# Kernel optimization log

Hardware: AMD Instinct MI355X
Metric: run time of the kernel (lower is better)

The kernel has to match this reference:

```python
import jax, jax.numpy as jnp
import numpy as np

REGION1 = REGION2 = 64
OVERLAP1 = OVERLAP2 = 0
MAX_M1 = MAX_M2 = 16


def dht1(x, axis):
    # 1D discrete Hartley transform along `axis` (real - imag of FFT)
    X = jnp.fft.fft(x, axis=axis)
    return X.real - X.imag


def dht2(x):
    # 2D DHT over last two axes
    X = jnp.fft.fft2(x, axes=(-2, -1))
    return X.real - X.imag


def flip_periodic2(x):
    # Faithful to torch code: flatten last two dims jointly, keep element 0, flip the rest
    s = x.shape
    n = s[-2] * s[-1]
    xf = x.reshape(s[:-2] + (n,))
    zf = jnp.concatenate([xf[..., :1], xf[..., 1:][..., ::-1]], axis=-1)
    return zf.reshape(s)


def hartley_conv2(x, y):
    # x: [b, i, h, w], y: [i, o, h, w] -> [b, o, h, w]; conv via Hartley theorem then idht
    X = dht2(x)
    Y = dht2(y)
    Xf = flip_periodic2(X)
    Yf = flip_periodic2(Y)
    Ye = 0.5 * (Y + Yf)
    Yo = 0.5 * (Y - Yf)
    Z = jnp.einsum('bihw,iohw->bohw', X, Ye) + jnp.einsum('bihw,iohw->bohw', Xf, Yo)
    n = x.shape[-2] * x.shape[-1]
    return dht2(Z) / n  # idht2 (DHT is involutory up to 1/n)


def spectral_conv2d(x, error_np, weights):
    B, Cin, S1, S2 = x.shape
    Cout = weights.shape[1]
    stride1 = REGION1 - OVERLAP1
    stride2 = REGION2 - OVERLAP2
    nr1 = (S1 - OVERLAP1) // stride1 + (1 if (S1 - OVERLAP1) % stride1 else 0)
    nr2 = (S2 - OVERLAP2) // stride2 + (1 if (S2 - OVERLAP2) % stride2 else 0)
    out = jnp.zeros((B, Cout, S1, S2), x.dtype)
    counts = np.zeros((S1, S2), np.float32)
    for i in range(nr1):
        for j in range(nr2):
            s1 = i * stride1; e1 = s1 + REGION1
            if e1 > S1:
                e1 = S1; s1 = max(e1 - REGION1, 0)
            s2 = j * stride2; e2 = s2 + REGION2
            if e2 > S2:
                e2 = S2; s2 = max(e2 - REGION2, 0)
            region_x = x[:, :, s1:e1, s2:e2]
            # adaptive per-sample mode counts from error signal (static, numpy)
            avg = error_np[:, s1:e1, s2:e2].mean(axis=(1, 2))
            mn, mx = avg.min(), avg.max()
            norm = (avg - mn) / (mx - mn) if (mx - mn) > 1e-8 else np.zeros_like(avg)
            nm1 = np.minimum((norm * (MAX_M1 - 1)).astype(np.int64) + 1, MAX_M1)
            nm2 = np.minimum((norm * (MAX_M2 - 1)).astype(np.int64) + 1, MAX_M2)
            # separable per-axis DHT of the region
            region_ht = dht1(dht1(region_x, -2), -1)
            out_ht = jnp.zeros((B, Cout, REGION1, REGION2), x.dtype)
            for b in range(B):
                n1 = int(nm1[b]); n2 = int(nm2[b])
                blk = hartley_conv2(region_ht[b:b + 1, :, :n1, :n2], weights[:, :, :n1, :n2])
                out_ht = out_ht.at[b, :, :n1, :n2].set(blk[0])
            # separable inverse per-axis DHT: dht1 along each axis / region area
            region_out = dht1(dht1(out_ht, -2), -1) / (REGION1 * REGION2)
            out = out.at[:, :, s1:e1, s2:e2].add(region_out)
            counts[s1:e1, s2:e2] += 1
    counts[counts == 0] = 1
    return out / jnp.asarray(counts, x.dtype)


def setup_inputs() -> dict:
    key = jax.random.key(0)
    k1, k2, k3 = jax.random.split(key, 3)
    B, Cin, Cout, S = 8, 32, 32, 256
    scale = 1.0 / (Cin * Cout)
    x = jax.random.normal(k1, (B, Cin, S, S), dtype=jnp.float32)
    error_signal = jax.random.uniform(k2, (B, S, S), dtype=jnp.float32)
    weights = scale * jax.random.uniform(k3, (Cin, Cout, MAX_M1, MAX_M2), dtype=jnp.float32)
    return {"x": x, "error_signal": error_signal, "weights": weights}


def reference(x, error_signal, weights):
    error_np = np.asarray(error_signal)
    return spectral_conv2d(x, error_np, weights)
```

## Files before the change

kernel.cpp:

```cpp
#include <hip/hip_runtime.h>
#include <math.h>

#define NB 8
#define CIN 32
#define COUT 32
#define SS 256
#define REG 64
#define NMAX 16

#define AVG_OFF   0
#define C64_OFF   4096
#define CN_OFF    4352
#define Y_OFF     8192
#define YF_OFF    (8u << 20)
#define XE_OFF    (16u << 20)
#define XO_OFF    (20u << 20)

__device__ __forceinline__ int region_n(const float* __restrict__ avg, int r, int b) {
    float mn = avg[r * 8], mx = mn;
    for (int bb = 1; bb < NB; ++bb) {
        float v = avg[r * 8 + bb];
        mn = fminf(mn, v);
        mx = fmaxf(mx, v);
    }
    float d = mx - mn;
    bool ok = ((double)d > 1e-8);
    float norm = ok ? (avg[r * 8 + b] - mn) / d : 0.0f;
    float tt = norm * 15.0f;
    int nv = (int)tt + 1;
    return nv > NMAX ? NMAX : nv;
}

__global__ void k_prep(const float* __restrict__ err, const float* __restrict__ wts,
                       float* __restrict__ avg, float* __restrict__ cyc64,
                       float* __restrict__ cycN, float* __restrict__ Y,
                       float* __restrict__ Yf) {
    int bx = blockIdx.x;
    int t = threadIdx.x;

    if (bx < 128) {
        int r = bx & 15, b = bx >> 4;
        int ri = r >> 2, rj = r & 3;
        const float* base = err + ((size_t)b * SS + ri * REG) * SS + rj * REG;
        double s = 0.0;
        for (int it = 0; it < 16; ++it) {
            int u = it * 4 + (t >> 6);
            int v = t & 63;
            s += (double)base[(size_t)u * SS + v];
        }
        __shared__ double sm[256];
        sm[t] = s;
        __syncthreads();
        for (int w = 128; w > 0; w >>= 1) {
            if (t < w) sm[t] += sm[t + w];
            __syncthreads();
        }
        if (t == 0) avg[r * 8 + b] = (float)(sm[0] / 4096.0);
        return;
    }

    if (bx == 128) {
        if (t < 64) {
            double a = (2.0 * M_PI / 64.0) * (double)t;
            cyc64[t] = (float)(cos(a) + sin(a));
        } else if (t < 64 + 136) {
            int e = t - 64;
            int n = 1;
            while (n * (n + 1) / 2 <= e) ++n;
            int j = e - n * (n - 1) / 2;
            double a = (2.0 * M_PI / (double)n) * (double)j;
            cycN[e] = (float)(cos(a) + sin(a));
        }
        return;
    }

    int io = bx - 129;
    __shared__ float Wt[256];
    __shared__ float T1[256];
    __shared__ float T2[256];
    __shared__ float cnAll[136];
    if (t < 136) {
        int e = t;
        int n = 1;
        while (n * (n + 1) / 2 <= e) ++n;
        int j = e - n * (n - 1) / 2;
        double a = (2.0 * M_PI / (double)n) * (double)j;
        cnAll[e] = (float)(cos(a) + sin(a));
    }
    Wt[t] = wts[(size_t)io * 256 + t];
    __syncthreads();

    for (int n = 1; n <= NMAX; ++n) {
        int nn = n * n;
        const float* cnL = &cnAll[(n * (n - 1)) / 2];
        int p = 0, q = 0;
        if (t < nn) { p = t / n; q = t - p * n; }
        if (t < nn) {
            float acc = 0.f;
            int idx = 0;
            for (int v = 0; v < n; ++v) {
                acc += Wt[p * 16 + v] * cnL[idx];
                idx += q; if (idx >= n) idx -= n;
            }
            T1[p * n + q] = acc;
        }
        __syncthreads();
        if (t < nn) {
            float acc = 0.f;
            int idx = 0;
            for (int u = 0; u < n; ++u) {
                acc += T1[u * n + q] * cnL[idx];
                idx += p; if (idx >= n) idx -= n;
            }
            T2[t] = acc;
        }
        __syncthreads();
        if (t < nn) {
            int pf = (p == 0) ? 0 : n - p;
            int qf = (q == 0) ? 0 : n - q;
            float v = 0.5f * (T2[p * n + q] + T2[pf * n + q] + T2[p * n + qf] - T2[pf * n + qf]);
            int m = n - 1;
            int ps2 = m * (m + 1) * (2 * m + 1) / 6;
            size_t basei = (size_t)1024 * ps2 + (size_t)io * nn;
            Y[basei + t] = v;
            int fk = (t == 0) ? 0 : nn - t;
            Yf[basei + fk] = v;
        }
        __syncthreads();
    }
}

__global__ void k_fwd(const float* __restrict__ x, const float* __restrict__ avg,
                      const float* __restrict__ cyc64, const float* __restrict__ cycN,
                      float* __restrict__ Xe, float* __restrict__ Xo) {
    int i = blockIdx.x, r = blockIdx.y, b = blockIdx.z;
    int n = region_n(avg, r, b);
    int nn = n * n;
    int ri = r >> 2, rj = r & 3;
    int t = threadIdx.x;

    __shared__ __align__(16) float R[64 * 64];
    __shared__ __align__(16) float M1[16 * 68];
    __shared__ float H[256];
    __shared__ float T1[256];
    __shared__ float T2[256];
    __shared__ float cyc64L[64];
    __shared__ float cnL[16];

    if (t < 64) cyc64L[t] = cyc64[t];
    if (t < n)  cnL[t] = cycN[(n * (n - 1)) / 2 + t];

    const float* base = x + (((size_t)(b * CIN + i)) * SS + ri * REG) * SS + rj * REG;
    float4* R4 = (float4*)R;
    {
        int u0 = t >> 4, c4 = t & 15;
        for (int it = 0; it < 4; ++it) {
            int u = it * 16 + u0;
            R4[u * 16 + c4] = *(const float4*)(base + (size_t)u * SS + c4 * 4);
        }
    }
    __syncthreads();

    {
        int uq = t >> 6, ps = (t >> 4) & 3, vg = t & 15;
        int p0 = ps, p1 = ps + 4, p2 = ps + 8, p3 = ps + 12;
        int i0 = (p0 * (uq << 4)) & 63;
        int i1 = (p1 * (uq << 4)) & 63;
        int i2 = (p2 * (uq << 4)) & 63;
        int i3 = (p3 * (uq << 4)) & 63;
        float4 a0 = {0.f,0.f,0.f,0.f}, a1 = a0, a2 = a0, a3 = a0;
        int ubase = (uq << 4) * 16 + vg;
        for (int uu = 0; uu < 16; ++uu) {
            float4 rv = R4[ubase + uu * 16];
            if (p0 < n) { float c = cyc64L[i0];
                a0.x += c*rv.x; a0.y += c*rv.y; a0.z += c*rv.z; a0.w += c*rv.w; }
            if (p1 < n) { float c = cyc64L[i1];
                a1.x += c*rv.x; a1.y += c*rv.y; a1.z += c*rv.z; a1.w += c*rv.w; }
            if (p2 < n) { float c = cyc64L[i2];
                a2.x += c*rv.x; a2.y += c*rv.y; a2.z += c*rv.z; a2.w += c*rv.w; }
            if (p3 < n) { float c = cyc64L[i3];
                a3.x += c*rv.x; a3.y += c*rv.y; a3.z += c*rv.z; a3.w += c*rv.w; }
            i0 = (i0 + p0) & 63; i1 = (i1 + p1) & 63;
            i2 = (i2 + p2) & 63; i3 = (i3 + p3) & 63;
        }
        __syncthreads();
        float4* P4 = R4;
        int pb = (uq << 8) + vg;
        if (p0 < n) P4[pb + p0 * 16] = a0;
        if (p1 < n) P4[pb + p1 * 16] = a1;
        if (p2 < n) P4[pb + p2 * 16] = a2;
        if (p3 < n) P4[pb + p3 * 16] = a3;
        __syncthreads();
        int pr = t >> 4, vr = t & 15;
        if (pr < n) {
            float4 q0 = P4[pr * 16 + vr];
            float4 q1 = P4[256 + pr * 16 + vr];
            float4 q2 = P4[512 + pr * 16 + vr];
            float4 q3 = P4[768 + pr * 16 + vr];
            float4 s;
            s.x = (q0.x + q1.x) + (q2.x + q3.x);
            s.y = (q0.y + q1.y) + (q2.y + q3.y);
            s.z = (q0.z + q1.z) + (q2.z + q3.z);
            s.w = (q0.w + q1.w) + (q2.w + q3.w);
            *(float4*)&M1[pr * 68 + vr * 4] = s;
        }
    }
    __syncthreads();

    int p = 0, q = 0;
    if (t < nn) { p = t / n; q = t - p * n; }

    if (t < nn) {
        float acc = 0.f;
        int idx = 0;
        for (int v = 0; v < 64; ++v) {
            acc += M1[p * 68 + v] * cyc64L[idx];
            idx = (idx + q) & 63;
        }
        H[t] = acc;
    }
    __syncthreads();

    if (t < nn) {
        float acc = 0.f;
        int idx = 0;
        for (int v = 0; v < n; ++v) {
            acc += H[p * n + v] * cnL[idx];
            idx += q; if (idx >= n) idx -= n;
        }
        T1[p * n + q] = acc;
    }
    __syncthreads();
    if (t < nn) {
        float acc = 0.f;
        int idx = 0;
        for (int u = 0; u < n; ++u) {
            acc += T1[u * n + q] * cnL[idx];
            idx += p; if (idx >= n) idx -= n;
        }
        T2[t] = acc;
    }
    __syncthreads();
    if (t < nn) {
        int pf = (p == 0) ? 0 : n - p;
        int qf = (q == 0) ? 0 : n - q;
        H[t] = 0.5f * (T2[p * n + q] + T2[pf * n + q] + T2[p * n + qf] - T2[pf * n + qf]);
    }
    __syncthreads();

    if (t < nn) {
        int fk = (t == 0) ? 0 : nn - t;
        float a = H[t], c = H[fk];
        size_t o = (((size_t)(b * 16 + r)) * CIN + i) * 256 + t;
        Xe[o] = 0.5f * (a + c);
        Xo[o] = 0.5f * (a - c);
    }
}

__global__ void k_zout(const float* __restrict__ Xe, const float* __restrict__ Xo,
                       const float* __restrict__ Y, const float* __restrict__ Yf,
                       const float* __restrict__ avg, const float* __restrict__ cyc64,
                       const float* __restrict__ cycN, float* __restrict__ out) {
    int og = blockIdx.x * 4;
    int br = blockIdx.y;
    int b = br >> 4, r = br & 15;
    int n = region_n(avg, r, b);
    int nn = n * n;
    int t = threadIdx.x;

    __shared__ float zbuf[4][256];
    __shared__ float T1[256];
    __shared__ float T2[256];
    __shared__ float Bk[256];
    __shared__ __align__(16) float E1[16 * 64];
    __shared__ __align__(16) float CTo[16 * 16 * 4];
    __shared__ float cyc64L[64];
    __shared__ float cnL[16];

    if (t < 64) cyc64L[t] = cyc64[t];
    if (t < n)  cnL[t] = cycN[(n * (n - 1)) / 2 + t];
    __syncthreads();

    {
        int pp = t >> 4, u0 = t & 15;
        float4 c;
        c.x = cyc64L[(pp * u0) & 63];
        c.y = cyc64L[(pp * (u0 + 16)) & 63];
        c.z = cyc64L[(pp * (u0 + 32)) & 63];
        c.w = cyc64L[(pp * (u0 + 48)) & 63];
        *(float4*)&CTo[t * 4] = c;
    }

    if (t < nn) {
        int m = n - 1;
        int ps2 = m * (m + 1) * (2 * m + 1) / 6;
        const float* Yb  = Y  + (size_t)1024 * ps2;
        const float* Yfb = Yf + (size_t)1024 * ps2;
        float a0 = 0.f, a1 = 0.f, a2 = 0.f, a3 = 0.f;
        size_t xbase = (size_t)br * CIN * 256;
        for (int i = 0; i < CIN; ++i) {
            float xe = Xe[xbase + i * 256 + t];
            float xo = Xo[xbase + i * 256 + t];
            const float* yp  = Yb  + (size_t)(i * COUT + og) * nn + t;
            const float* yfp = Yfb + (size_t)(i * COUT + og) * nn + t;
            a0 += xe * yp[0]      + xo * yfp[0];
            a1 += xe * yp[nn]     + xo * yfp[nn];
            a2 += xe * yp[2 * nn] + xo * yfp[2 * nn];
            a3 += xe * yp[3 * nn] + xo * yfp[3 * nn];
        }
        zbuf[0][t] = a0; zbuf[1][t] = a1; zbuf[2][t] = a2; zbuf[3][t] = a3;
    }

    int p = 0, q = 0;
    if (t < nn) { p = t / n; q = t - p * n; }
    int ri = r >> 2, rj = r & 3;
    int u0 = t >> 4, vg = t & 15;
    const float4* E14 = (const float4*)E1;
    const float4* CT4 = (const float4*)CTo;
    const float inv = 1.0f / 4096.0f;

    for (int oo = 0; oo < 4; ++oo) {
        __syncthreads();
        if (t < nn) {
            float acc = 0.f;
            int idx = 0;
            for (int v = 0; v < n; ++v) {
                acc += zbuf[oo][p * n + v] * cnL[idx];
                idx += q; if (idx >= n) idx -= n;
            }
            T1[p * n + q] = acc;
        }
        __syncthreads();
        if (t < nn) {
            float acc = 0.f;
            int idx = 0;
            for (int u = 0; u < n; ++u) {
                acc += T1[u * n + q] * cnL[idx];
                idx += p; if (idx >= n) idx -= n;
            }
            T2[t] = acc;
        }
        __syncthreads();
        if (t < nn) {
            int pf = (p == 0) ? 0 : n - p;
            int qf = (q == 0) ? 0 : n - q;
            Bk[t] = 0.5f * (T2[p * n + q] + T2[pf * n + q] + T2[p * n + qf] - T2[pf * n + qf])
                    / (float)nn;
        }
        __syncthreads();
        for (int mm = t; mm < n * 64; mm += 256) {
            int pp = mm >> 6, v = mm & 63;
            float acc = 0.f;
            int idx = 0;
            for (int qq = 0; qq < n; ++qq) {
                acc += Bk[pp * n + qq] * cyc64L[idx];
                idx = (idx + v) & 63;
            }
            E1[pp * 64 + v] = acc;
        }
        __syncthreads();
        float* ob = out + (((size_t)(b * COUT + og + oo)) * SS + ri * REG) * SS + rj * REG;
        float4 aA = {0.f,0.f,0.f,0.f}, aB = aA, aC = aA, aD = aA;
        for (int pp = 0; pp < n; ++pp) {
            float4 e = E14[pp * 16 + vg];
            float4 c = CT4[pp * 16 + u0];
            aA.x += c.x*e.x; aA.y += c.x*e.y; aA.z += c.x*e.z; aA.w += c.x*e.w;
            aB.x += c.y*e.x; aB.y += c.y*e.y; aB.z += c.y*e.z; aB.w += c.y*e.w;
            aC.x += c.z*e.x; aC.y += c.z*e.y; aC.z += c.z*e.z; aC.w += c.z*e.w;
            aD.x += c.w*e.x; aD.y += c.w*e.y; aD.z += c.w*e.z; aD.w += c.w*e.w;
        }
        aA.x *= inv; aA.y *= inv; aA.z *= inv; aA.w *= inv;
        aB.x *= inv; aB.y *= inv; aB.z *= inv; aB.w *= inv;
        aC.x *= inv; aC.y *= inv; aC.z *= inv; aC.w *= inv;
        aD.x *= inv; aD.y *= inv; aD.z *= inv; aD.w *= inv;
        *(float4*)(ob + (size_t)(u0)      * SS + vg * 4) = aA;
        *(float4*)(ob + (size_t)(16 + u0) * SS + vg * 4) = aB;
        *(float4*)(ob + (size_t)(32 + u0) * SS + vg * 4) = aC;
        *(float4*)(ob + (size_t)(48 + u0) * SS + vg * 4) = aD;
    }
}

extern "C" void kernel_launch(void* const* d_in, const int* in_sizes, int n_in,
                              void* d_out, int out_size, void* d_ws, size_t ws_size,
                              hipStream_t stream) {
    const float* x   = (const float*)d_in[0];
    const float* err = (const float*)d_in[1];
    const float* wts = (const float*)d_in[2];
    float* out = (float*)d_out;
    char* ws = (char*)d_ws;

    float* avg   = (float*)(ws + AVG_OFF);
    float* cyc64 = (float*)(ws + C64_OFF);
    float* cycN  = (float*)(ws + CN_OFF);
    float* Y     = (float*)(ws + Y_OFF);
    float* Yf    = (float*)(ws + YF_OFF);
    float* Xe    = (float*)(ws + XE_OFF);
    float* Xo    = (float*)(ws + XO_OFF);

    k_prep<<<dim3(128 + 1 + CIN * COUT), 256, 0, stream>>>(err, wts, avg, cyc64, cycN, Y, Yf);
    k_fwd<<<dim3(CIN, 16, NB), 256, 0, stream>>>(x, avg, cyc64, cycN, Xe, Xo);
    k_zout<<<dim3(8, 128), 256, 0, stream>>>(Xe, Xo, Y, Yf, avg, cyc64, cycN, out);
}
```

Baseline: 181.2 us.

## Assign one output channel per block and split channel reduction across threads

The zout kernel now launches one block per output channel (32 instead of 8 groups of 4). The input-channel contraction is split across four thread groups that each cover 8 channels, with partial sums reduced in shared memory, so all 256 threads take part rather than only the n*n active ones. The aim is more parallelism and shorter serial loops per block. In exchange, Xe/Xo are re-read for every output channel and the CTo cosine table setup is repeated in four times as many blocks.

```diff
diff --git a/kernel.cpp b/kernel.cpp
--- a/kernel.cpp
+++ b/kernel.cpp
@@ -261,14 +261,15 @@
                        const float* __restrict__ Y, const float* __restrict__ Yf,
                        const float* __restrict__ avg, const float* __restrict__ cyc64,
                        const float* __restrict__ cycN, float* __restrict__ out) {
-    int og = blockIdx.x * 4;
+    int o  = blockIdx.x;
     int br = blockIdx.y;
     int b = br >> 4, r = br & 15;
     int n = region_n(avg, r, b);
     int nn = n * n;
     int t = threadIdx.x;
 
-    __shared__ float zbuf[4][256];
+    __shared__ float zpart[4][256];
+    __shared__ float Zs[256];
     __shared__ float T1[256];
     __shared__ float T2[256];
     __shared__ float Bk[256];
@@ -279,6 +280,33 @@
 
     if (t < 64) cyc64L[t] = cyc64[t];
     if (t < n)  cnL[t] = cycN[(n * (n - 1)) / 2 + t];
+
+    int ig = t >> 6, k0 = t & 63;
+    {
+        int m = n - 1;
+        int ps2 = m * (m + 1) * (2 * m + 1) / 6;
+        const float* Yb  = Y  + (size_t)1024 * ps2;
+        const float* Yfb = Yf + (size_t)1024 * ps2;
+        size_t xb = (size_t)br * CIN * 256;
+        float a0 = 0.f, a1 = 0.f, a2 = 0.f, a3 = 0.f;
+        int k1 = k0 + 64, k2 = k0 + 128, k3 = k0 + 192;
+#pragma unroll 2
+        for (int ii = 0; ii < 8; ++ii) {
+            int i = ig * 8 + ii;
+            const float* xep = Xe + xb + (size_t)i * 256;
+            const float* xop = Xo + xb + (size_t)i * 256;
+            const float* yp  = Yb  + (size_t)(i * COUT + o) * nn;
+            const float* yfp = Yfb + (size_t)(i * COUT + o) * nn;
+            if (k0 < nn) a0 += xep[k0] * yp[k0] + xop[k0] * yfp[k0];
+            if (k1 < nn) a1 += xep[k1] * yp[k1] + xop[k1] * yfp[k1];
+            if (k2 < nn) a2 += xep[k2] * yp[k2] + xop[k2] * yfp[k2];
+            if (k3 < nn) a3 += xep[k3] * yp[k3] + xop[k3] * yfp[k3];
+        }
+        zpart[ig][k0]  = a0;
+        zpart[ig][k1]  = a1;
+        zpart[ig][k2]  = a2;
+        zpart[ig][k3]  = a3;
+    }
     __syncthreads();
 
     {
@@ -290,94 +318,76 @@
         c.w = cyc64L[(pp * (u0 + 48)) & 63];
         *(float4*)&CTo[t * 4] = c;
     }
-
-    if (t < nn) {
-        int m = n - 1;
-        int ps2 = m * (m + 1) * (2 * m + 1) / 6;
-        const float* Yb  = Y  + (size_t)1024 * ps2;
-        const float* Yfb = Yf + (size_t)1024 * ps2;
-        float a0 = 0.f, a1 = 0.f, a2 = 0.f, a3 = 0.f;
-        size_t xbase = (size_t)br * CIN * 256;
-        for (int i = 0; i < CIN; ++i) {
-            float xe = Xe[xbase + i * 256 + t];
-            float xo = Xo[xbase + i * 256 + t];
-            const float* yp  = Yb  + (size_t)(i * COUT + og) * nn + t;
-            const float* yfp = Yfb + (size_t)(i * COUT + og) * nn + t;
-            a0 += xe * yp[0]      + xo * yfp[0];
-            a1 += xe * yp[nn]     + xo * yfp[nn];
-            a2 += xe * yp[2 * nn] + xo * yfp[2 * nn];
-            a3 += xe * yp[3 * nn] + xo * yfp[3 * nn];
-        }
-        zbuf[0][t] = a0; zbuf[1][t] = a1; zbuf[2][t] = a2; zbuf[3][t] = a3;
-    }
+    if (t < nn)
+        Zs[t] = (zpart[0][t] + zpart[1][t]) + (zpart[2][t] + zpart[3][t]);
 
     int p = 0, q = 0;
     if (t < nn) { p = t / n; q = t - p * n; }
+    __syncthreads();
+
+    if (t < nn) {
+        float acc = 0.f;
+        int idx = 0;
+        for (int v = 0; v < n; ++v) {
+            acc += Zs[p * n + v] * cnL[idx];
+            idx += q; if (idx >= n) idx -= n;
+        }
+        T1[p * n + q] = acc;
+    }
+    __syncthreads();
+    if (t < nn) {
+        float acc = 0.f;
+        int idx = 0;
+        for (int u = 0; u < n; ++u) {
+            acc += T1[u * n + q] * cnL[idx];
+            idx += p; if (idx >= n) idx -= n;
+        }
+        T2[t] = acc;
+    }
+    __syncthreads();
+    if (t < nn) {
+        int pf = (p == 0) ? 0 : n - p;
+        int qf = (q == 0) ? 0 : n - q;
+        Bk[t] = 0.5f * (T2[p * n + q] + T2[pf * n + q] + T2[p * n + qf] - T2[pf * n + qf])
+                / (float)nn;
+    }
+    __syncthreads();
+
+    for (int mm = t; mm < n * 64; mm += 256) {
+        int pp = mm >> 6, v = mm & 63;
+        float acc = 0.f;
+        int idx = 0;
+        for (int qq = 0; qq < n; ++qq) {
+            acc += Bk[pp * n + qq] * cyc64L[idx];
+            idx = (idx + v) & 63;
+        }
+        E1[pp * 64 + v] = acc;
+    }
+    __syncthreads();
+
     int ri = r >> 2, rj = r & 3;
-    int u0 = t >> 4, vg = t & 15;
+    float* ob = out + (((size_t)(b * COUT + o)) * SS + ri * REG) * SS + rj * REG;
     const float4* E14 = (const float4*)E1;
     const float4* CT4 = (const float4*)CTo;
     const float inv = 1.0f / 4096.0f;
-
-    for (int oo = 0; oo < 4; ++oo) {
-        __syncthreads();
-        if (t < nn) {
-            float acc = 0.f;
-            int idx = 0;
-            for (int v = 0; v < n; ++v) {
-                acc += zbuf[oo][p * n + v] * cnL[idx];
-                idx += q; if (idx >= n) idx -= n;
-            }
-            T1[p * n + q] = acc;
-        }
-        __syncthreads();
-        if (t < nn) {
-            float acc = 0.f;
-            int idx = 0;
-            for (int u = 0; u < n; ++u) {
-                acc += T1[u * n + q] * cnL[idx];
-                idx += p; if (idx >= n) idx -= n;
-            }
-            T2[t] = acc;
-        }
-        __syncthreads();
-        if (t < nn) {
-            int pf = (p == 0) ? 0 : n - p;
-            int qf = (q == 0) ? 0 : n - q;
-            Bk[t] = 0.5f * (T2[p * n + q] + T2[pf * n + q] + T2[p * n + qf] - T2[pf * n + qf])
-                    / (float)nn;
-        }
-        __syncthreads();
-        for (int mm = t; mm < n * 64; mm += 256) {
-            int pp = mm >> 6, v = mm & 63;
-            float acc = 0.f;
-            int idx = 0;
-            for (int qq = 0; qq < n; ++qq) {
-                acc += Bk[pp * n + qq] * cyc64L[idx];
-                idx = (idx + v) & 63;
-            }
-            E1[pp * 64 + v] = acc;
-        }
-        __syncthreads();
-        float* ob = out + (((size_t)(b * COUT + og + oo)) * SS + ri * REG) * SS + rj * REG;
-        float4 aA = {0.f,0.f,0.f,0.f}, aB = aA, aC = aA, aD = aA;
-        for (int pp = 0; pp < n; ++pp) {
-            float4 e = E14[pp * 16 + vg];
-            float4 c = CT4[pp * 16 + u0];
-            aA.x += c.x*e.x; aA.y += c.x*e.y; aA.z += c.x*e.z; aA.w += c.x*e.w;
-            aB.x += c.y*e.x; aB.y += c.y*e.y; aB.z += c.y*e.z; aB.w += c.y*e.w;
-            aC.x += c.z*e.x; aC.y += c.z*e.y; aC.z += c.z*e.z; aC.w += c.z*e.w;
-            aD.x += c.w*e.x; aD.y += c.w*e.y; aD.z += c.w*e.z; aD.w += c.w*e.w;
-        }
-        aA.x *= inv; aA.y *= inv; aA.z *= inv; aA.w *= inv;
-        aB.x *= inv; aB.y *= inv; aB.z *= inv; aB.w *= inv;
-        aC.x *= inv; aC.y *= inv; aC.z *= inv; aC.w *= inv;
-        aD.x *= inv; aD.y *= inv; aD.z *= inv; aD.w *= inv;
-        *(float4*)(ob + (size_t)(u0)      * SS + vg * 4) = aA;
-        *(float4*)(ob + (size_t)(16 + u0) * SS + vg * 4) = aB;
-        *(float4*)(ob + (size_t)(32 + u0) * SS + vg * 4) = aC;
-        *(float4*)(ob + (size_t)(48 + u0) * SS + vg * 4) = aD;
-    }
+    int u0 = t >> 4, vg = t & 15;
+    float4 aA = {0.f,0.f,0.f,0.f}, aB = aA, aC = aA, aD = aA;
+    for (int pp = 0; pp < n; ++pp) {
+        float4 e = E14[pp * 16 + vg];
+        float4 c = CT4[pp * 16 + u0];
+        aA.x += c.x*e.x; aA.y += c.x*e.y; aA.z += c.x*e.z; aA.w += c.x*e.w;
+        aB.x += c.y*e.x; aB.y += c.y*e.y; aB.z += c.y*e.z; aB.w += c.y*e.w;
+        aC.x += c.z*e.x; aC.y += c.z*e.y; aC.z += c.z*e.z; aC.w += c.z*e.w;
+        aD.x += c.w*e.x; aD.y += c.w*e.y; aD.z += c.w*e.z; aD.w += c.w*e.w;
+    }
+    aA.x *= inv; aA.y *= inv; aA.z *= inv; aA.w *= inv;
+    aB.x *= inv; aB.y *= inv; aB.z *= inv; aB.w *= inv;
+    aC.x *= inv; aC.y *= inv; aC.z *= inv; aC.w *= inv;
+    aD.x *= inv; aD.y *= inv; aD.z *= inv; aD.w *= inv;
+    *(float4*)(ob + (size_t)(u0)      * SS + vg * 4) = aA;
+    *(float4*)(ob + (size_t)(16 + u0) * SS + vg * 4) = aB;
+    *(float4*)(ob + (size_t)(32 + u0) * SS + vg * 4) = aC;
+    *(float4*)(ob + (size_t)(48 + u0) * SS + vg * 4) = aD;
 }
 
 extern "C" void kernel_launch(void* const* d_in, const int* in_sizes, int n_in,
@@ -399,5 +409,5 @@
 
     k_prep<<<dim3(128 + 1 + CIN * COUT), 256, 0, stream>>>(err, wts, avg, cyc64, cycN, Y, Yf);
     k_fwd<<<dim3(CIN, 16, NB), 256, 0, stream>>>(x, avg, cyc64, cycN, Xe, Xo);
-    k_zout<<<dim3(8, 128), 256, 0, stream>>>(Xe, Xo, Y, Yf, avg, cyc64, cycN, out);
+    k_zout<<<dim3(COUT, 128), 256, 0, stream>>>(Xe, Xo, Y, Yf, avg, cyc64, cycN, out);
 }
```

After: 186.0 us. 2.6% more time.
